# Kernel tuning notes

Hardware: AMD Instinct MI355X
Metric: run time of the kernel (lower is better)

## Reference

```python
import jax, jax.numpy as jnp
import numpy as np

FRAMESIZE = 80


def setup_inputs() -> dict:
    key = jax.random.key(0)
    k1, k2 = jax.random.split(key)
    B, t, nbands = 32, 4000, 257
    H = jax.random.normal(k1, (B, t, nbands), dtype=jnp.float32)
    noise_u = jax.random.uniform(k2, (B, t, FRAMESIZE), dtype=jnp.float32)
    return {"H": H, "noise_u": noise_u}


def reference(H, noise_u):
    """Time-varying filtered noise via linear-phase LTV-FIR + overlap-add.

    H       : [B, t, nbands] half spectrum (real) of zero-phase filter
    noise_u : [B, t, framesize] uniform noise in [0, 1)
    returns : [B, t*framesize]
    """
    framesize = FRAMESIZE
    B, t, nbands = H.shape
    N = 2 * nbands - 1  # FIR length L (odd)

    # torch.hann_window default is periodic: w[n] = 0.5*(1 - cos(2*pi*n/N))
    hann = (0.5 * (1.0 - jnp.cos(2.0 * jnp.pi * jnp.arange(N) / N))).astype(jnp.float32)

    # zero-phase impulse response -> linear phase via circular shift, then window
    zero_phase = jnp.fft.irfft(H, n=N, axis=-1)              # [B, t, N]
    lin_phase = jnp.roll(zero_phase, nbands - 1, axis=-1)    # [B, t, N]
    firwin = lin_phase * hann                                # [B, t, N]
    L = N

    noise = noise_u * 2.0 - 1.0                              # uniform in [-1, 1)

    # full linear convolution per (B, t) frame via FFT (fftconvolve, mode='full')
    nfft = framesize + L - 1
    Fn = jnp.fft.rfft(noise, n=nfft, axis=-1)
    Ff = jnp.fft.rfft(firwin, n=nfft, axis=-1)
    filtered = jnp.fft.irfft(Fn * Ff, n=nfft, axis=-1)       # [B, t, framesize+L-1]

    # overlap-add with hop = framesize (the conv_transpose1d(eye) trick, done as
    # a direct strided scatter-add), then trim the L-1 tail as in the original
    out_len = t * framesize + L - 1
    idx = (jnp.arange(t)[:, None] * framesize + jnp.arange(nfft)[None, :]).reshape(-1)
    out = jnp.zeros((B, out_len), dtype=filtered.dtype)
    out = out.at[:, idx].add(filtered.reshape(B, -1))
    return out[:, : t * framesize]
```

## Files before the change

kernel.cpp:

```cpp
#include <hip/hip_runtime.h>
#include <stdint.h>

typedef unsigned short u16;
typedef unsigned int   u32;
typedef __attribute__((ext_vector_type(8))) short short8;
typedef __attribute__((ext_vector_type(4))) float f32x4;

#define TPB 256
#define FPB 64
#define NB 257
#define LF 513
#define FS 80
#define NCH 9
#define MT_TOTAL 33
#define HROW 296
#define FROW 536
#define TAB_ELEMS (MT_TOTAL*NCH*64*8)

__device__ __forceinline__ u32 f2bf(float f){
  u32 u = __float_as_uint(f);
  return (u + 0x7fffu + ((u >> 16) & 1u)) >> 16;
}
#define BF2LO(u) __uint_as_float((u) << 16)
#define BF2HI(u) __uint_as_float((u) & 0xffff0000u)

__global__ void build_table(u16* __restrict__ tab){
  int id = blockIdx.x * blockDim.x + threadIdx.x;
  if (id >= TAB_ELEMS) return;
  int j    = id & 7;
  int lane = (id >> 3) & 63;
  int cc   = (id >> 9) % NCH;
  int mt   = (id >> 9) / NCH;
  int tap  = mt * 16 + (lane & 15);
  int kslot= cc * 32 + (lane >> 4) * 8 + j;
  float val = 0.f;
  if (tap < LF){
    float hann = 0.5f - 0.5f * cosf(6.28318530717958647f * (float)tap / 513.f);
    if (kslot < 256){
      int k  = kslot + 1;
      int rr = (k * (tap + 257)) % 513;
      val = (2.f / 513.f) * hann * cosf((float)rr * (6.28318530717958647f / 513.f));
    } else if (kslot == 256){
      val = hann * (1.f / 513.f);
    }
  }
  tab[id] = (u16)f2bf(val);
}

__launch_bounds__(TPB, 2)
__global__ void fused(const float* __restrict__ Hg, const float* __restrict__ noiseg,
                      const u16* __restrict__ tab, float* __restrict__ out, int outTotal){
  __shared__ u16 uSh[FPB * FROW];
  __shared__ u16 noiseSh[FPB * FS];

  const int tid  = threadIdx.x;
  const int lane = tid & 63;
  const int w    = tid >> 6;
  const int ln15 = lane & 15;
  const int q    = lane >> 4;
  const int blk  = blockIdx.x;
  const int f0   = blk * FPB;

  u16* Hlds = uSh;

  #pragma unroll
  for (int e = 0; e < 32; ++e){
    int id = tid + TPB * e;
    int r = id >> 7, p = id & 127;
    const float* gp = Hg + (size_t)(f0 + r) * NB + 1 + 2 * p;
    u32 lo = f2bf(gp[0]), hi = f2bf(gp[1]);
    *(u32*)&Hlds[r * HROW + 2 * p] = lo | (hi << 16);
  }
  if (tid < 64){
    *(u32*)&Hlds[tid * HROW + 256] = f2bf(Hg[(size_t)(f0 + tid) * NB]);
  }
  #pragma unroll
  for (int e = 0; e < 5; ++e){
    int id = tid + TPB * e;
    if (id < 64 * 19){
      int r = id / 19, c2 = id % 19;
      *(u32*)&Hlds[r * HROW + 258 + 2 * c2] = 0u;
    }
  }
  #pragma unroll
  for (int e = 0; e < 10; ++e){
    int id = tid + TPB * e;
    int r = id / 40, c2 = id % 40;
    float2 v = *(const float2*)(noiseg + (size_t)(f0 + r) * FS + 2 * c2);
    u32 lo = f2bf(v.x * 2.f - 1.f), hi = f2bf(v.y * 2.f - 1.f);
    *(u32*)&noiseSh[r * FS + 2 * c2] = lo | (hi << 16);
  }
  __syncthreads();

  const int mtBegin = (w == 0) ? 0 : (9 + 8 * (w - 1));
  const int mtCount = (w == 0) ? 9 : 8;
  f32x4 acc[9][4];
  #pragma unroll
  for (int a = 0; a < 9; ++a)
    #pragma unroll
    for (int b = 0; b < 4; ++b) acc[a][b] = (f32x4){0.f, 0.f, 0.f, 0.f};

  const short8* tab8 = (const short8*)tab;
  for (int c = 0; c < NCH; ++c){
    short8 bfrag[4];
    #pragma unroll
    for (int nt = 0; nt < 4; ++nt)
      bfrag[nt] = *(const short8*)&Hlds[(nt * 16 + ln15) * HROW + c * 32 + q * 8];
    #pragma unroll
    for (int mt = 0; mt < 9; ++mt){
      if (mt < mtCount){
        short8 afrag = tab8[((mtBegin + mt) * NCH + c) * 64 + lane];
        #pragma unroll
        for (int nt = 0; nt < 4; ++nt)
          acc[mt][nt] = __builtin_amdgcn_mfma_f32_16x16x32_bf16(afrag, bfrag[nt], acc[mt][nt], 0, 0, 0);
      }
    }
  }
  __syncthreads();

  u16* fir = uSh;
  #pragma unroll
  for (int mt = 0; mt < 9; ++mt){
    if (mt < mtCount){
      int tap0 = (mtBegin + mt) * 16 + q * 4;
      #pragma unroll
      for (int nt = 0; nt < 4; ++nt){
        int frame = nt * 16 + ln15;
        f32x4 v = acc[mt][nt];
        uint2 pk;
        pk.x = f2bf(v.x) | (f2bf(v.y) << 16);
        pk.y = f2bf(v.z) | (f2bf(v.w) << 16);
        *(uint2*)&fir[frame * FROW + 8 + tap0] = pk;
      }
    }
  }
  if (tid < 256){
    int r = tid >> 2, s = tid & 3;
    ((u32*)&fir[r * FROW])[s] = 0u;
  }
  __syncthreads();

  for (int task = tid; task < 704; task += TPB){
    int s0 = blk * (FPB * FS) + task * 8;
    if (s0 >= outTotal) continue;
    int qb = s0 / 320000;
    int fA = max(f0, qb * 4000);
    int fB = min(f0 + FPB, qb * 4000 + 4000);
    int fLo = max(fA, (s0 >= 512) ? (s0 - 512) / 80 : 0);
    int fHi = min(fB - 1, (s0 + 7) / 80);
    float ac[8];
    #pragma unroll
    for (int r = 0; r < 8; ++r) ac[r] = 0.f;

    for (int f = fLo; f <= fHi; ++f){
      int frel = f - f0;
      int j0 = s0 - 80 * f;
      const u16* frow = uSh + frel * FROW + 8;
      const u16* nrow = noiseSh + frel * FS;
      int gLo = (j0 > 512) ? ((j0 - 512) >> 2) : 0;
      int gHi = min(19, (j0 >> 2) + 1);
      float F[12];
      int x = j0 - 4 * gLo;
      uint2 q1 = *(const uint2*)(frow + x);
      uint2 q2 = *(const uint2*)(frow + x + 4);
      F[4] = BF2LO(q1.x); F[5] = BF2HI(q1.x); F[6]  = BF2LO(q1.y); F[7]  = BF2HI(q1.y);
      F[8] = BF2LO(q2.x); F[9] = BF2HI(q2.x); F[10] = BF2LO(q2.y); F[11] = BF2HI(q2.y);
      for (int g = gLo; g <= gHi; ++g){
        uint2 q0 = *(const uint2*)(frow + (j0 - 4 * g - 4));
        F[0] = BF2LO(q0.x); F[1] = BF2HI(q0.x); F[2] = BF2LO(q0.y); F[3] = BF2HI(q0.y);
        uint2 nq = *(const uint2*)(nrow + 4 * g);
        float n0 = BF2LO(nq.x), n1 = BF2HI(nq.x), n2 = BF2LO(nq.y), n3 = BF2HI(nq.y);
        #pragma unroll
        for (int r = 0; r < 8; ++r){
          ac[r] = fmaf(n0, F[4 + r], ac[r]);
          ac[r] = fmaf(n1, F[3 + r], ac[r]);
          ac[r] = fmaf(n2, F[2 + r], ac[r]);
          ac[r] = fmaf(n3, F[1 + r], ac[r]);
        }
        F[8] = F[4]; F[9] = F[5]; F[10] = F[6]; F[11] = F[7];
        F[4] = F[0]; F[5] = F[1]; F[6]  = F[2]; F[7]  = F[3];
      }
    }
    if (task >= 64 && task < 640){
      float4 v0 = make_float4(ac[0], ac[1], ac[2], ac[3]);
      float4 v1 = make_float4(ac[4], ac[5], ac[6], ac[7]);
      *(float4*)&out[s0]     = v0;
      *(float4*)&out[s0 + 4] = v1;
    } else if (fLo <= fHi){
      #pragma unroll
      for (int r = 0; r < 8; ++r) atomicAdd(&out[s0 + r], ac[r]);
    }
  }
}

extern "C" void kernel_launch(void* const* d_in, const int* in_sizes, int n_in,
                              void* d_out, int out_size, void* d_ws, size_t ws_size,
                              hipStream_t stream){
  const float* Hg     = (const float*)d_in[0];
  const float* noiseg = (const float*)d_in[1];
  float* out = (float*)d_out;
  u16* tab = (u16*)d_ws;

  hipMemsetAsync(d_out, 0, (size_t)out_size * sizeof(float), stream);
  build_table<<<TAB_ELEMS / TPB, TPB, 0, stream>>>(tab);
  fused<<<(32 * 4000) / FPB, TPB, 0, stream>>>(Hg, noiseg, tab, out, out_size);
}
```

Baseline: 557.9 us.

## Switch to fp16 with packed dot2 convolution, smaller blocks, reversed FIR layout

Switches the FIR-synthesis GEMM from bf16 to fp16 MFMA. It replaces the scalar fp32 FMA overlap-add convolution with packed fp16 dot2 instructions over a reversed FIR layout in shared memory. Blocks shrink to 32 frames and 192 threads with 3 waves per SIMD, and each thread now produces 16 outputs, with a fixed per-thread frame/offset schedule instead of per-task bounds computation. The packed dot2 path should cut VALU work in the convolution, which likely dominated, at the cost of fp16 range and precision risks and more atomics at block edges.

```diff
diff --git a/kernel.cpp b/kernel.cpp
--- a/kernel.cpp
+++ b/kernel.cpp
@@ -3,26 +3,34 @@
 
 typedef unsigned short u16;
 typedef unsigned int   u32;
-typedef __attribute__((ext_vector_type(8))) short short8;
+typedef _Float16 f16;
+typedef __attribute__((ext_vector_type(2))) _Float16 half2v;
+typedef __attribute__((ext_vector_type(8))) _Float16 half8;
 typedef __attribute__((ext_vector_type(4))) float f32x4;
 
-#define TPB 256
-#define FPB 64
+#define TPB 192
+#define FPB 32
 #define NB 257
 #define LF 513
 #define FS 80
 #define NCH 9
 #define MT_TOTAL 33
-#define HROW 296
-#define FROW 536
+#define HROW16 296
+#define GROW 346
+#define NROW 44
 #define TAB_ELEMS (MT_TOTAL*NCH*64*8)
 
-__device__ __forceinline__ u32 f2bf(float f){
-  u32 u = __float_as_uint(f);
-  return (u + 0x7fffu + ((u >> 16) & 1u)) >> 16;
-}
-#define BF2LO(u) __uint_as_float((u) << 16)
-#define BF2HI(u) __uint_as_float((u) & 0xffff0000u)
+__device__ __forceinline__ u32 pk2(float a, float b){
+  return __builtin_bit_cast(u32, __builtin_amdgcn_cvt_pkrtz(a, b));
+}
+__device__ __forceinline__ float dot2(u32 a, u32 b, float c){
+#if __has_builtin(__builtin_amdgcn_fdot2)
+  return __builtin_amdgcn_fdot2(__builtin_bit_cast(half2v, a), __builtin_bit_cast(half2v, b), c, false);
+#else
+  half2v x = __builtin_bit_cast(half2v, a), y = __builtin_bit_cast(half2v, b);
+  return fmaf((float)x[1], (float)y[1], fmaf((float)x[0], (float)y[0], c));
+#endif
+}
 
 __global__ void build_table(u16* __restrict__ tab){
   int id = blockIdx.x * blockDim.x + threadIdx.x;
@@ -36,22 +44,22 @@
   float val = 0.f;
   if (tap < LF){
     float hann = 0.5f - 0.5f * cosf(6.28318530717958647f * (float)tap / 513.f);
-    if (kslot < 256){
-      int k  = kslot + 1;
-      int rr = (k * (tap + 257)) % 513;
+    if (kslot == 0){
+      val = hann * (1.f / 513.f);
+    } else if (kslot <= 256){
+      int rr = (kslot * (tap + 257)) % 513;
       val = (2.f / 513.f) * hann * cosf((float)rr * (6.28318530717958647f / 513.f));
-    } else if (kslot == 256){
-      val = hann * (1.f / 513.f);
-    }
-  }
-  tab[id] = (u16)f2bf(val);
-}
-
-__launch_bounds__(TPB, 2)
+    }
+  }
+  f16 h = (f16)val;
+  tab[id] = __builtin_bit_cast(u16, h);
+}
+
+__launch_bounds__(TPB, 3)
 __global__ void fused(const float* __restrict__ Hg, const float* __restrict__ noiseg,
-                      const u16* __restrict__ tab, float* __restrict__ out, int outTotal){
-  __shared__ u16 uSh[FPB * FROW];
-  __shared__ u16 noiseSh[FPB * FS];
+                      const u16* __restrict__ tab, float* __restrict__ out){
+  __shared__ __align__(16) u32 Gu[FPB * GROW];
+  __shared__ __align__(16) u32 Nu[FPB * NROW];
 
   const int tid  = threadIdx.x;
   const int lane = tid & 63;
@@ -61,134 +69,137 @@
   const int blk  = blockIdx.x;
   const int f0   = blk * FPB;
 
-  u16* Hlds = uSh;
-
-  #pragma unroll
-  for (int e = 0; e < 32; ++e){
+  u16* Hlds = (u16*)Gu;
+
+  #pragma unroll
+  for (int e = 0; e < 24; ++e){
     int id = tid + TPB * e;
-    int r = id >> 7, p = id & 127;
-    const float* gp = Hg + (size_t)(f0 + r) * NB + 1 + 2 * p;
-    u32 lo = f2bf(gp[0]), hi = f2bf(gp[1]);
-    *(u32*)&Hlds[r * HROW + 2 * p] = lo | (hi << 16);
-  }
-  if (tid < 64){
-    *(u32*)&Hlds[tid * HROW + 256] = f2bf(Hg[(size_t)(f0 + tid) * NB]);
-  }
-  #pragma unroll
-  for (int e = 0; e < 5; ++e){
+    int r = id / 144, p = id % 144;
+    const float* gp = Hg + (size_t)(f0 + r) * NB;
+    u32 v = 0u;
+    if (p < 128)       v = pk2(gp[2*p], gp[2*p+1]);
+    else if (p == 128) v = pk2(gp[256], 0.f);
+    *(u32*)&Hlds[r * HROW16 + 2 * p] = v;
+  }
+  #pragma unroll
+  for (int e = 0; e < 7; ++e){
     int id = tid + TPB * e;
-    if (id < 64 * 19){
-      int r = id / 19, c2 = id % 19;
-      *(u32*)&Hlds[r * HROW + 258 + 2 * c2] = 0u;
-    }
-  }
-  #pragma unroll
-  for (int e = 0; e < 10; ++e){
+    if (id < FPB * 40){
+      int r = id / 40, m = id % 40;
+      const float* np = noiseg + (size_t)(f0 + r) * FS + 2 * m;
+      Nu[r * NROW + m] = pk2(np[0] * 2.f - 1.f, np[1] * 2.f - 1.f);
+    }
+  }
+  if (tid < FPB){
+    float n0 = noiseg[(size_t)(f0 + tid) * FS] * 2.f - 1.f;
+    Nu[tid * NROW + 40] = 0u;
+    Nu[tid * NROW + 41] = pk2(0.f, n0);
+    Nu[tid * NROW + 42] = 0u;
+    Nu[tid * NROW + 43] = 0u;
+  }
+  __syncthreads();
+
+  f32x4 acc[11][2];
+  #pragma unroll
+  for (int a = 0; a < 11; ++a){ acc[a][0] = (f32x4){0,0,0,0}; acc[a][1] = (f32x4){0,0,0,0}; }
+  const half8* tab8 = (const half8*)tab;
+  for (int c = 0; c < NCH; ++c){
+    half8 bfrag[2];
+    #pragma unroll
+    for (int nt = 0; nt < 2; ++nt)
+      bfrag[nt] = *(const half8*)&Hlds[(nt*16 + ln15) * HROW16 + c*32 + q*8];
+    #pragma unroll
+    for (int mm = 0; mm < 11; ++mm){
+      half8 afrag = tab8[((w*11 + mm) * NCH + c) * 64 + lane];
+      #pragma unroll
+      for (int nt = 0; nt < 2; ++nt)
+        acc[mm][nt] = __builtin_amdgcn_mfma_f32_16x16x32_f16(afrag, bfrag[nt], acc[mm][nt], 0, 0, 0);
+    }
+  }
+  __syncthreads();
+
+  #pragma unroll
+  for (int mm = 0; mm < 11; ++mm){
+    int t0 = (w*11 + mm)*16 + q*4;
+    #pragma unroll
+    for (int nt = 0; nt < 2; ++nt){
+      int frame = nt*16 + ln15;
+      f32x4 v = acc[mm][nt];
+      uint2 pk;
+      pk.x = pk2(v.w, v.z);
+      pk.y = pk2(v.y, v.x);
+      *(uint2*)&Gu[frame * GROW + (302 - (t0 >> 1))] = pk;
+    }
+  }
+  #pragma unroll
+  for (int e = 0; e < 14; ++e){
     int id = tid + TPB * e;
-    int r = id / 40, c2 = id % 40;
-    float2 v = *(const float2*)(noiseg + (size_t)(f0 + r) * FS + 2 * c2);
-    u32 lo = f2bf(v.x * 2.f - 1.f), hi = f2bf(v.y * 2.f - 1.f);
-    *(u32*)&noiseSh[r * FS + 2 * c2] = lo | (hi << 16);
+    if (id < FPB * 82){
+      int r = id / 82, s2 = id % 82;
+      Gu[r * GROW + (s2 < 40 ? s2 : 264 + s2)] = 0u;
+    }
   }
   __syncthreads();
 
-  const int mtBegin = (w == 0) ? 0 : (9 + 8 * (w - 1));
-  const int mtCount = (w == 0) ? 9 : 8;
-  f32x4 acc[9][4];
-  #pragma unroll
-  for (int a = 0; a < 9; ++a)
-    #pragma unroll
-    for (int b = 0; b < 4; ++b) acc[a][b] = (f32x4){0.f, 0.f, 0.f, 0.f};
-
-  const short8* tab8 = (const short8*)tab;
-  for (int c = 0; c < NCH; ++c){
-    short8 bfrag[4];
-    #pragma unroll
-    for (int nt = 0; nt < 4; ++nt)
-      bfrag[nt] = *(const short8*)&Hlds[(nt * 16 + ln15) * HROW + c * 32 + q * 8];
-    #pragma unroll
-    for (int mt = 0; mt < 9; ++mt){
-      if (mt < mtCount){
-        short8 afrag = tab8[((mtBegin + mt) * NCH + c) * 64 + lane];
+  const bool lastB = (blk % 125) == 124;
+  if (!(tid >= 160 && lastB)){
+    const int s    = tid % 5;
+    const int fTop = tid / 5;
+    const int dMax = (s <= 2) ? 7 : 6;
+    float ac[16];
+    #pragma unroll
+    for (int r = 0; r < 16; ++r) ac[r] = 0.f;
+
+    #pragma unroll 1
+    for (int d = 0; d <= 7; ++d){
+      const int frel = fTop - d;
+      if (d <= dMax && frel >= 0 && frel < FPB){
+        const u32* Gr = Gu + frel * GROW;
+        const u32* Nr = Nu + frel * NROW;
+        const int V = 304 - 8*s - 40*d;
+        u32 W[12];
+        { uint2 a0 = *(const uint2*)(Gr + V - 8);
+          uint2 a1 = *(const uint2*)(Gr + V - 6);
+          uint2 a2 = *(const uint2*)(Gr + V - 4);
+          uint2 a3 = *(const uint2*)(Gr + V - 2);
+          W[0]=a0.x; W[1]=a0.y; W[2]=a1.x; W[3]=a1.y; W[4]=a2.x; W[5]=a2.y; W[6]=a3.x; W[7]=a3.y; }
+        const u32 n0hi = Nr[41];
         #pragma unroll
-        for (int nt = 0; nt < 4; ++nt)
-          acc[mt][nt] = __builtin_amdgcn_mfma_f32_16x16x32_bf16(afrag, bfrag[nt], acc[mt][nt], 0, 0, 0);
+        for (int k = 0; k < 8; ++k)
+          ac[2*k] = dot2(n0hi, W[7-k], ac[2*k]);
+        uint4 naNext = *(const uint4*)(Nr);
+        #pragma unroll
+        for (int c = 0; c < 10; ++c){
+          uint2 g0 = *(const uint2*)(Gr + V + 4*c);
+          uint2 g1 = *(const uint2*)(Gr + V + 4*c + 2);
+          W[8] = g0.x; W[9] = g0.y; W[10] = g1.x; W[11] = g1.y;
+          uint4 naCur = naNext;
+          naNext = *(const uint4*)(Nr + 4*c + 4);
+          u32 nAv[5] = {naCur.x, naCur.y, naCur.z, naCur.w, naNext.x};
+          #pragma unroll
+          for (int i = 0; i < 4; ++i){
+            u32 a   = nAv[i];
+            u32 sft = __builtin_amdgcn_alignbit(nAv[i+1], nAv[i], 16);
+            #pragma unroll
+            for (int k = 0; k < 8; ++k){
+              ac[2*k]   = dot2(sft, W[i+8-k], ac[2*k]);
+              ac[2*k+1] = dot2(a,   W[i+7-k], ac[2*k+1]);
+            }
+          }
+          #pragma unroll
+          for (int p = 0; p < 8; ++p) W[p] = W[p+4];
+        }
       }
     }
-  }
-  __syncthreads();
-
-  u16* fir = uSh;
-  #pragma unroll
-  for (int mt = 0; mt < 9; ++mt){
-    if (mt < mtCount){
-      int tap0 = (mtBegin + mt) * 16 + q * 4;
+    const size_t s0 = (size_t)blk * 2560 + (size_t)tid * 16;
+    if (tid >= 32 && tid < 160){
+      *(float4*)&out[s0]      = make_float4(ac[0], ac[1], ac[2], ac[3]);
+      *(float4*)&out[s0 + 4]  = make_float4(ac[4], ac[5], ac[6], ac[7]);
+      *(float4*)&out[s0 + 8]  = make_float4(ac[8], ac[9], ac[10], ac[11]);
+      *(float4*)&out[s0 + 12] = make_float4(ac[12], ac[13], ac[14], ac[15]);
+    } else {
       #pragma unroll
-      for (int nt = 0; nt < 4; ++nt){
-        int frame = nt * 16 + ln15;
-        f32x4 v = acc[mt][nt];
-        uint2 pk;
-        pk.x = f2bf(v.x) | (f2bf(v.y) << 16);
-        pk.y = f2bf(v.z) | (f2bf(v.w) << 16);
-        *(uint2*)&fir[frame * FROW + 8 + tap0] = pk;
-      }
-    }
-  }
-  if (tid < 256){
-    int r = tid >> 2, s = tid & 3;
-    ((u32*)&fir[r * FROW])[s] = 0u;
-  }
-  __syncthreads();
-
-  for (int task = tid; task < 704; task += TPB){
-    int s0 = blk * (FPB * FS) + task * 8;
-    if (s0 >= outTotal) continue;
-    int qb = s0 / 320000;
-    int fA = max(f0, qb * 4000);
-    int fB = min(f0 + FPB, qb * 4000 + 4000);
-    int fLo = max(fA, (s0 >= 512) ? (s0 - 512) / 80 : 0);
-    int fHi = min(fB - 1, (s0 + 7) / 80);
-    float ac[8];
-    #pragma unroll
-    for (int r = 0; r < 8; ++r) ac[r] = 0.f;
-
-    for (int f = fLo; f <= fHi; ++f){
-      int frel = f - f0;
-      int j0 = s0 - 80 * f;
-      const u16* frow = uSh + frel * FROW + 8;
-      const u16* nrow = noiseSh + frel * FS;
-      int gLo = (j0 > 512) ? ((j0 - 512) >> 2) : 0;
-      int gHi = min(19, (j0 >> 2) + 1);
-      float F[12];
-      int x = j0 - 4 * gLo;
-      uint2 q1 = *(const uint2*)(frow + x);
-      uint2 q2 = *(const uint2*)(frow + x + 4);
-      F[4] = BF2LO(q1.x); F[5] = BF2HI(q1.x); F[6]  = BF2LO(q1.y); F[7]  = BF2HI(q1.y);
-      F[8] = BF2LO(q2.x); F[9] = BF2HI(q2.x); F[10] = BF2LO(q2.y); F[11] = BF2HI(q2.y);
-      for (int g = gLo; g <= gHi; ++g){
-        uint2 q0 = *(const uint2*)(frow + (j0 - 4 * g - 4));
-        F[0] = BF2LO(q0.x); F[1] = BF2HI(q0.x); F[2] = BF2LO(q0.y); F[3] = BF2HI(q0.y);
-        uint2 nq = *(const uint2*)(nrow + 4 * g);
-        float n0 = BF2LO(nq.x), n1 = BF2HI(nq.x), n2 = BF2LO(nq.y), n3 = BF2HI(nq.y);
-        #pragma unroll
-        for (int r = 0; r < 8; ++r){
-          ac[r] = fmaf(n0, F[4 + r], ac[r]);
-          ac[r] = fmaf(n1, F[3 + r], ac[r]);
-          ac[r] = fmaf(n2, F[2 + r], ac[r]);
-          ac[r] = fmaf(n3, F[1 + r], ac[r]);
-        }
-        F[8] = F[4]; F[9] = F[5]; F[10] = F[6]; F[11] = F[7];
-        F[4] = F[0]; F[5] = F[1]; F[6]  = F[2]; F[7]  = F[3];
-      }
-    }
-    if (task >= 64 && task < 640){
-      float4 v0 = make_float4(ac[0], ac[1], ac[2], ac[3]);
-      float4 v1 = make_float4(ac[4], ac[5], ac[6], ac[7]);
-      *(float4*)&out[s0]     = v0;
-      *(float4*)&out[s0 + 4] = v1;
-    } else if (fLo <= fHi){
-      #pragma unroll
-      for (int r = 0; r < 8; ++r) atomicAdd(&out[s0 + r], ac[r]);
+      for (int r = 0; r < 16; ++r) atomicAdd(&out[s0 + r], ac[r]);
     }
   }
 }
@@ -202,6 +213,6 @@
   u16* tab = (u16*)d_ws;
 
   hipMemsetAsync(d_out, 0, (size_t)out_size * sizeof(float), stream);
-  build_table<<<TAB_ELEMS / TPB, TPB, 0, stream>>>(tab);
-  fused<<<(32 * 4000) / FPB, TPB, 0, stream>>>(Hg, noiseg, tab, out, out_size);
-}
+  build_table<<<TAB_ELEMS / 256, 256, 0, stream>>>(tab);
+  fused<<<(32 * 4000) / FPB, TPB, 0, stream>>>(Hg, noiseg, tab, out);
+}
```

New measurement: 660.9 us. 1.18x slower.
